# Optimization experiments

Measured on AMD Instinct MI355X. Metric: run time of the kernel, lower is better.

Reference implementation:

```python
import jax, jax.numpy as jnp
import numpy as np

B, N, D = 4, 2048, 1024
H = 16
E = D // H  # 64


def setup_inputs() -> dict:
    key = jax.random.key(0)
    k1, k2, k3 = jax.random.split(key, 3)
    x = jax.random.normal(k1, (B, N, D), dtype=jnp.float32)
    W_qkv = jax.random.normal(k2, (D, 3 * D), dtype=jnp.float32) * 0.02
    W_o = jax.random.normal(k3, (D, D), dtype=jnp.float32) * 0.02
    return {"x": x, "W_qkv": W_qkv, "W_o": W_o}


def reference(x, W_qkv, W_o):
    b, n, d = x.shape
    # QKV projection, then split as 'b n (3 heads e) -> 3 b heads n e'
    qkv = (x @ W_qkv).reshape(b, n, 3, H, E)
    qkv = jnp.transpose(qkv, (2, 0, 3, 1, 4))  # [3, b, H, n, E]
    q, k, v = qkv[0], qkv[1], qkv[2]
    # scores[i, j] = k_i . q_j / sqrt(E)  (note: rows indexed by k-pos, cols by q-pos, as in original)
    scores = jnp.einsum('bhie,bhje->bhij', k, q) / jnp.sqrt(jnp.asarray(E, dtype=x.dtype))
    # original masks strictly-lower-triangular (i > j) entries to -inf
    keep = jnp.triu(jnp.ones((n, n), dtype=bool))  # True where i <= j
    scores = jnp.where(keep, scores, -jnp.inf)
    attn = jax.nn.softmax(scores, axis=-1)  # softmax over last (q/v) axis, as in original
    out = jnp.einsum('bhij,bhje->bhie', attn, v)  # [b, H, n, E]
    out = jnp.transpose(out, (0, 2, 1, 3)).reshape(b, n, H * E)
    return out @ W_o
```

## Files before the change

### kernel.cpp

```cpp
#include <hip/hip_runtime.h>

typedef unsigned short u16;
typedef __bf16 bf16x8 __attribute__((ext_vector_type(8)));
typedef float f32x4 __attribute__((ext_vector_type(4)));
typedef unsigned short u16x8 __attribute__((ext_vector_type(8)));

__device__ inline u16 f2bf(float f) {
  unsigned u = __builtin_bit_cast(unsigned, f);
  u += 0x7fff + ((u >> 16) & 1);
  return (u16)(u >> 16);
}

__device__ inline f32x4 mfma16(bf16x8 a, bf16x8 b, f32x4 c) {
  return __builtin_amdgcn_mfma_f32_16x16x32_bf16(a, b, c, 0, 0, 0);
}

__global__ __launch_bounds__(256) void k_convert(const float* __restrict__ in,
                                                 u16* __restrict__ out, int n8) {
  int i = blockIdx.x * 256 + threadIdx.x;
  if (i >= n8) return;
  const float4* p = (const float4*)in + 2 * (size_t)i;
  float4 a = p[0], b = p[1];
  u16x8 v;
  v[0] = f2bf(a.x); v[1] = f2bf(a.y); v[2] = f2bf(a.z); v[3] = f2bf(a.w);
  v[4] = f2bf(b.x); v[5] = f2bf(b.y); v[6] = f2bf(b.z); v[7] = f2bf(b.w);
  *((u16x8*)out + i) = v;
}

__global__ __launch_bounds__(256) void k_transpose_conv(const float* __restrict__ in,
                                                        u16* __restrict__ out, int R, int C) {
  __shared__ float t[32][33];
  int c0 = blockIdx.x * 32, r0 = blockIdx.y * 32;
  int lx = threadIdx.x, ly = threadIdx.y;
#pragma unroll
  for (int i = 0; i < 32; i += 8)
    t[ly + i][lx] = in[(size_t)(r0 + ly + i) * C + c0 + lx];
  __syncthreads();
#pragma unroll
  for (int i = 0; i < 32; i += 8)
    out[(size_t)(c0 + ly + i) * R + r0 + lx] = f2bf(t[lx][ly + i]);
}

__global__ __launch_bounds__(256) void k_transpose_v(const u16* __restrict__ V,
                                                     u16* __restrict__ Vt) {
  __shared__ u16 t[64][72];
  int bh = blockIdx.y, n0 = blockIdx.x * 64;
  int tid = threadIdx.x;
  const u16* src = V + (size_t)bh * 2048 * 64;
  u16* dst = Vt + (size_t)bh * 64 * 2048;
#pragma unroll
  for (int half = 0; half < 2; ++half) {
    int f = half * 2048 + tid * 8;
    int r = f >> 6, e = f & 63;
    *(u16x8*)&t[r][e] = *(const u16x8*)&src[(size_t)(n0 + r) * 64 + e];
  }
  __syncthreads();
#pragma unroll
  for (int half = 0; half < 2; ++half) {
    int f = half * 2048 + tid * 8;
    int e = f >> 6, c = f & 63;
    u16x8 v;
#pragma unroll
    for (int j = 0; j < 8; ++j) v[j] = t[c + j][e];
    *(u16x8*)&dst[(size_t)e * 2048 + n0 + c] = v;
  }
}

template <int EPI>
__global__ __launch_bounds__(256) void k_gemm(const u16* __restrict__ A,
                                              const u16* __restrict__ Bt,
                                              void* __restrict__ o0, void* __restrict__ o1,
                                              void* __restrict__ o2, int M, int N, int K) {
  __shared__ u16 Al[2][128 * 40];
  __shared__ u16 Bl[2][128 * 40];
  const int tid = threadIdx.x, lane = tid & 63;
  const int row0 = blockIdx.x * 128, col0 = blockIdx.y * 128;
  const int w = tid >> 6;
  const int wr = (w >> 1) * 64, wc = (w & 1) * 64;
  const int srow = tid >> 2, skk = (tid & 3) * 8;
  const int l15 = lane & 15, lk = (lane >> 4) * 8;
  const int NK = K >> 5;
  f32x4 acc[4][4] = {};
  u16x8 ra0, ra1, rb0, rb1;
  const u16* ap0 = A + (size_t)(row0 + srow) * K + skk;
  const u16* bp0 = Bt + (size_t)(col0 + srow) * K + skk;

#define GLOAD(kt)                                              \
  do {                                                         \
    const u16* ap = ap0 + (size_t)(kt) * 32;                   \
    ra0 = *(const u16x8*)ap;                                   \
    ra1 = *(const u16x8*)(ap + (size_t)64 * K);                \
    const u16* bp = bp0 + (size_t)(kt) * 32;                   \
    rb0 = *(const u16x8*)bp;                                   \
    rb1 = *(const u16x8*)(bp + (size_t)64 * K);                \
  } while (0)
#define SWRITE(buf)                                            \
  do {                                                         \
    *(u16x8*)&Al[buf][srow * 40 + skk] = ra0;                  \
    *(u16x8*)&Al[buf][(64 + srow) * 40 + skk] = ra1;           \
    *(u16x8*)&Bl[buf][srow * 40 + skk] = rb0;                  \
    *(u16x8*)&Bl[buf][(64 + srow) * 40 + skk] = rb1;           \
  } while (0)

  GLOAD(0);
  SWRITE(0);
  int cur = 0;
  for (int kt = 0; kt < NK; ++kt) {
    __syncthreads();
    if (kt + 1 < NK) GLOAD(kt + 1);
    bf16x8 af[4], bfr[4];
#pragma unroll
    for (int m = 0; m < 4; ++m)
      af[m] = *(const bf16x8*)&Al[cur][(wr + m * 16 + l15) * 40 + lk];
#pragma unroll
    for (int n = 0; n < 4; ++n)
      bfr[n] = *(const bf16x8*)&Bl[cur][(wc + n * 16 + l15) * 40 + lk];
#pragma unroll
    for (int m = 0; m < 4; ++m)
#pragma unroll
      for (int n = 0; n < 4; ++n) acc[m][n] = mfma16(af[m], bfr[n], acc[m][n]);
    if (kt + 1 < NK) {
      SWRITE(cur ^ 1);
      cur ^= 1;
    }
  }
#undef GLOAD
#undef SWRITE
#pragma unroll
  for (int m = 0; m < 4; ++m)
#pragma unroll
    for (int n = 0; n < 4; ++n)
#pragma unroll
      for (int r = 0; r < 4; ++r) {
        int gr = row0 + wr + m * 16 + (lane >> 4) * 4 + r;
        int gc = col0 + wc + n * 16 + l15;
        float v = acc[m][n][r];
        if (EPI == 0) {
          int t = gc >> 10, rem = gc & 1023;
          int h = rem >> 6, e = rem & 63;
          int b = gr >> 11, nn = gr & 2047;
          if (t == 1) v *= 0.18033688011112042f;
          u16* dst = (t == 0) ? (u16*)o0 : (t == 1) ? (u16*)o1 : (u16*)o2;
          dst[((size_t)(b * 16 + h) * 2048 + nn) * 64 + e] = f2bf(v);
        } else {
          ((float*)o0)[(size_t)gr * N + gc] = v;
        }
      }
}

__global__ __launch_bounds__(256, 4) void k_attn(const u16* __restrict__ Kg,
                                                 const u16* __restrict__ Qg,
                                                 const u16* __restrict__ Vtg,
                                                 u16* __restrict__ Og) {
  __shared__ u16 Kq[64][72];
  __shared__ u16 Vt[64][72];
  __shared__ u16 Pl[4][32][80];
  const int tid = threadIdx.x, lane = tid & 63, w = tid >> 6;
  const int l15 = lane & 15, lg = lane >> 4;
  const int r0 = (15 - (int)blockIdx.x) * 128;
  const int bh = blockIdx.y;
  const int wrow = r0 + w * 32;
  const size_t base = (size_t)bh * 2048 * 64;

  bf16x8 qf[2][2];
#pragma unroll
  for (int i0 = 0; i0 < 2; ++i0)
#pragma unroll
    for (int kk = 0; kk < 2; ++kk)
      qf[i0][kk] = *(const bf16x8*)&Kg[base + (size_t)(wrow + i0 * 16 + l15) * 64 + kk * 32 + lg * 8];

  f32x4 acc[2][4] = {};
  float s_part[2][4] = {};

  const int srow = tid >> 2;
  const int scol = (tid & 3) * 16;
  const u16* kp = Qg + base + (size_t)srow * 64 + scol;
  const u16* vp = Vtg + base + (size_t)srow * 2048 + scol;

  u16x8 kr0, kr1, vr0, vr1;
  kr0 = *(const u16x8*)(kp + (size_t)r0 * 64);
  kr1 = *(const u16x8*)(kp + (size_t)r0 * 64 + 8);
  vr0 = *(const u16x8*)(vp + r0);
  vr1 = *(const u16x8*)(vp + r0 + 8);

  for (int j0 = r0; j0 < 2048; j0 += 64) {
    __syncthreads();
    *(u16x8*)&Kq[srow][scol] = kr0;
    *(u16x8*)&Kq[srow][scol + 8] = kr1;
    *(u16x8*)&Vt[srow][scol] = vr0;
    *(u16x8*)&Vt[srow][scol + 8] = vr1;
    __syncthreads();
    int jn = (j0 + 64 < 2048) ? j0 + 64 : j0;
    kr0 = *(const u16x8*)(kp + (size_t)jn * 64);
    kr1 = *(const u16x8*)(kp + (size_t)jn * 64 + 8);
    vr0 = *(const u16x8*)(vp + jn);
    vr1 = *(const u16x8*)(vp + jn + 8);

    if (j0 + 63 < wrow) continue;
    const bool diag = (j0 < wrow + 32);

    f32x4 S[2][4];
#pragma unroll
    for (int jf = 0; jf < 4; ++jf) {
      bf16x8 kf0 = *(const bf16x8*)&Kq[jf * 16 + l15][lg * 8];
      bf16x8 kf1 = *(const bf16x8*)&Kq[jf * 16 + l15][32 + lg * 8];
#pragma unroll
      for (int i0 = 0; i0 < 2; ++i0) {
        f32x4 z = {};
        z = mfma16(qf[i0][0], kf0, z);
        z = mfma16(qf[i0][1], kf1, z);
        S[i0][jf] = z;
      }
    }

#pragma unroll
    for (int i0 = 0; i0 < 2; ++i0)
#pragma unroll
      for (int r = 0; r < 4; ++r) {
        int gi = wrow + i0 * 16 + lg * 4 + r;
        float p0 = __builtin_amdgcn_exp2f(S[i0][0][r]);
        float p1 = __builtin_amdgcn_exp2f(S[i0][1][r]);
        float p2 = __builtin_amdgcn_exp2f(S[i0][2][r]);
        float p3 = __builtin_amdgcn_exp2f(S[i0][3][r]);
        if (diag) {
          p0 = (j0 + l15 >= gi) ? p0 : 0.f;
          p1 = (j0 + 16 + l15 >= gi) ? p1 : 0.f;
          p2 = (j0 + 32 + l15 >= gi) ? p2 : 0.f;
          p3 = (j0 + 48 + l15 >= gi) ? p3 : 0.f;
        }
        s_part[i0][r] += (p0 + p1) + (p2 + p3);
        u16* prow = &Pl[w][i0 * 16 + lg * 4 + r][l15];
        prow[0] = f2bf(p0);
        prow[16] = f2bf(p1);
        prow[32] = f2bf(p2);
        prow[48] = f2bf(p3);
      }

    bf16x8 pa[2][2];
#pragma unroll
    for (int i0 = 0; i0 < 2; ++i0) {
      pa[i0][0] = *(const bf16x8*)&Pl[w][i0 * 16 + l15][lg * 8];
      pa[i0][1] = *(const bf16x8*)&Pl[w][i0 * 16 + l15][32 + lg * 8];
    }
#pragma unroll
    for (int ef = 0; ef < 4; ++ef) {
      bf16x8 vb0 = *(const bf16x8*)&Vt[ef * 16 + l15][lg * 8];
      bf16x8 vb1 = *(const bf16x8*)&Vt[ef * 16 + l15][32 + lg * 8];
#pragma unroll
      for (int i0 = 0; i0 < 2; ++i0) {
        acc[i0][ef] = mfma16(pa[i0][0], vb0, acc[i0][ef]);
        acc[i0][ef] = mfma16(pa[i0][1], vb1, acc[i0][ef]);
      }
    }
  }

#pragma unroll
  for (int i0 = 0; i0 < 2; ++i0)
#pragma unroll
    for (int r = 0; r < 4; ++r) {
      float s = s_part[i0][r];
#pragma unroll
      for (int d = 1; d < 16; d <<= 1) s += __shfl_xor(s, d);
      s_part[i0][r] = 1.0f / s;
    }
  const size_t obase = ((size_t)(bh >> 4) * 2048) * 1024 + (size_t)(bh & 15) * 64;
#pragma unroll
  for (int i0 = 0; i0 < 2; ++i0)
#pragma unroll
    for (int ef = 0; ef < 4; ++ef)
#pragma unroll
      for (int r = 0; r < 4; ++r) {
        int gi = wrow + i0 * 16 + lg * 4 + r;
        Og[obase + (size_t)gi * 1024 + ef * 16 + l15] = f2bf(acc[i0][ef][r] * s_part[i0][r]);
      }
}

extern "C" void kernel_launch(void* const* d_in, const int* in_sizes, int n_in,
                              void* d_out, int out_size, void* d_ws, size_t ws_size,
                              hipStream_t stream) {
  const float* x = (const float*)d_in[0];
  const float* Wqkv = (const float*)d_in[1];
  const float* Wo = (const float*)d_in[2];
  char* ws = (char*)d_ws;
  u16* x_bf = (u16*)(ws);
  u16* Wq_t = (u16*)(ws + 16777216);
  u16* Wo_t = (u16*)(ws + 23068672);
  u16* Q = (u16*)(ws + 25165824);
  u16* Kx = (u16*)(ws + 41943040);
  u16* V = (u16*)(ws + 58720256);
  u16* Vt = (u16*)(ws + 75497472);
  u16* O = (u16*)(ws + 92274688);

  k_convert<<<8192 * 1024 / 8 / 256, 256, 0, stream>>>(x, x_bf, 8192 * 1024 / 8);
  k_transpose_conv<<<dim3(3072 / 32, 1024 / 32), dim3(32, 8), 0, stream>>>(Wqkv, Wq_t, 1024, 3072);
  k_transpose_conv<<<dim3(1024 / 32, 1024 / 32), dim3(32, 8), 0, stream>>>(Wo, Wo_t, 1024, 1024);
  k_gemm<0><<<dim3(64, 24), 256, 0, stream>>>(x_bf, Wq_t, Q, Kx, V, 8192, 3072, 1024);
  k_transpose_v<<<dim3(32, 64), 256, 0, stream>>>(V, Vt);
  k_attn<<<dim3(16, 64), 256, 0, stream>>>(Kx, Q, Vt, O);
  k_gemm<1><<<dim3(64, 8), 256, 0, stream>>>(O, Wo_t, d_out, nullptr, nullptr, 8192, 1024, 1024);
}
```

Baseline: 290.7 us.

## Use async global-to-LDS loads in GEMM and vectorize permuted P stores in attention

The GEMM staging now uses global_load_lds to copy A/B tiles straight into unpadded LDS buffers, replacing the register round-trip and the separate LDS write step. The attention kernel stores P as packed 4-element vectors in a permuted column order. The V transpose kernel applies the matching permutation so the PV product is unchanged. The causal row-block order is also remapped per (batch, head) to spread long and short blocks across the GPU. Dropping the LDS row padding in the GEMM may add bank conflicts on the MFMA fragment reads.

After: 290.2 us. No clear change (-0.2%).

```diff
diff --git a/kernel.cpp b/kernel.cpp
--- a/kernel.cpp
+++ b/kernel.cpp
@@ -3,6 +3,7 @@
 typedef unsigned short u16;
 typedef __bf16 bf16x8 __attribute__((ext_vector_type(8)));
 typedef float f32x4 __attribute__((ext_vector_type(4)));
+typedef unsigned short u16x4 __attribute__((ext_vector_type(4)));
 typedef unsigned short u16x8 __attribute__((ext_vector_type(8)));
 
 __device__ inline u16 f2bf(float f) {
@@ -13,6 +14,11 @@
 
 __device__ inline f32x4 mfma16(bf16x8 a, bf16x8 b, f32x4 c) {
   return __builtin_amdgcn_mfma_f32_16x16x32_bf16(a, b, c, 0, 0, 0);
+}
+
+__device__ inline void async16(const u16* g, u16* l) {
+  __builtin_amdgcn_global_load_lds((const __attribute__((address_space(1))) void*)g,
+                                   (__attribute__((address_space(3))) void*)l, 16, 0, 0);
 }
 
 __global__ __launch_bounds__(256) void k_convert(const float* __restrict__ in,
@@ -61,7 +67,10 @@
     int e = f >> 6, c = f & 63;
     u16x8 v;
 #pragma unroll
-    for (int j = 0; j < 8; ++j) v[j] = t[c + j][e];
+    for (int j = 0; j < 8; ++j) {
+      int tt = c + j;
+      v[j] = t[16 * (tt & 3) + (tt >> 2)][e];
+    }
     *(u16x8*)&dst[(size_t)e * 2048 + n0 + c] = v;
   }
 }
@@ -71,61 +80,47 @@
                                               const u16* __restrict__ Bt,
                                               void* __restrict__ o0, void* __restrict__ o1,
                                               void* __restrict__ o2, int M, int N, int K) {
-  __shared__ u16 Al[2][128 * 40];
-  __shared__ u16 Bl[2][128 * 40];
+  __shared__ u16 Al[2][128 * 32];
+  __shared__ u16 Bl[2][128 * 32];
   const int tid = threadIdx.x, lane = tid & 63;
   const int row0 = blockIdx.x * 128, col0 = blockIdx.y * 128;
   const int w = tid >> 6;
   const int wr = (w >> 1) * 64, wc = (w & 1) * 64;
-  const int srow = tid >> 2, skk = (tid & 3) * 8;
   const int l15 = lane & 15, lk = (lane >> 4) * 8;
   const int NK = K >> 5;
   f32x4 acc[4][4] = {};
-  u16x8 ra0, ra1, rb0, rb1;
-  const u16* ap0 = A + (size_t)(row0 + srow) * K + skk;
-  const u16* bp0 = Bt + (size_t)(col0 + srow) * K + skk;
-
-#define GLOAD(kt)                                              \
-  do {                                                         \
-    const u16* ap = ap0 + (size_t)(kt) * 32;                   \
-    ra0 = *(const u16x8*)ap;                                   \
-    ra1 = *(const u16x8*)(ap + (size_t)64 * K);                \
-    const u16* bp = bp0 + (size_t)(kt) * 32;                   \
-    rb0 = *(const u16x8*)bp;                                   \
-    rb1 = *(const u16x8*)(bp + (size_t)64 * K);                \
+  const u16* ap0 = A + (size_t)(row0 + (tid >> 2)) * K + (tid & 3) * 8;
+  const u16* bp0 = Bt + (size_t)(col0 + (tid >> 2)) * K + (tid & 3) * 8;
+
+#define STAGE(kt, buf)                                       \
+  do {                                                       \
+    const u16* as = ap0 + (size_t)(kt) * 32;                 \
+    const u16* bs = bp0 + (size_t)(kt) * 32;                 \
+    async16(as, &Al[buf][tid * 8]);                          \
+    async16(as + (size_t)64 * K, &Al[buf][2048 + tid * 8]);  \
+    async16(bs, &Bl[buf][tid * 8]);                          \
+    async16(bs + (size_t)64 * K, &Bl[buf][2048 + tid * 8]);  \
   } while (0)
-#define SWRITE(buf)                                            \
-  do {                                                         \
-    *(u16x8*)&Al[buf][srow * 40 + skk] = ra0;                  \
-    *(u16x8*)&Al[buf][(64 + srow) * 40 + skk] = ra1;           \
-    *(u16x8*)&Bl[buf][srow * 40 + skk] = rb0;                  \
-    *(u16x8*)&Bl[buf][(64 + srow) * 40 + skk] = rb1;           \
-  } while (0)
-
-  GLOAD(0);
-  SWRITE(0);
+
+  STAGE(0, 0);
   int cur = 0;
   for (int kt = 0; kt < NK; ++kt) {
     __syncthreads();
-    if (kt + 1 < NK) GLOAD(kt + 1);
+    if (kt + 1 < NK) STAGE(kt + 1, cur ^ 1);
     bf16x8 af[4], bfr[4];
 #pragma unroll
     for (int m = 0; m < 4; ++m)
-      af[m] = *(const bf16x8*)&Al[cur][(wr + m * 16 + l15) * 40 + lk];
+      af[m] = *(const bf16x8*)&Al[cur][(wr + m * 16 + l15) * 32 + lk];
 #pragma unroll
     for (int n = 0; n < 4; ++n)
-      bfr[n] = *(const bf16x8*)&Bl[cur][(wc + n * 16 + l15) * 40 + lk];
+      bfr[n] = *(const bf16x8*)&Bl[cur][(wc + n * 16 + l15) * 32 + lk];
 #pragma unroll
     for (int m = 0; m < 4; ++m)
 #pragma unroll
       for (int n = 0; n < 4; ++n) acc[m][n] = mfma16(af[m], bfr[n], acc[m][n]);
-    if (kt + 1 < NK) {
-      SWRITE(cur ^ 1);
-      cur ^= 1;
-    }
-  }
-#undef GLOAD
-#undef SWRITE
+    cur ^= 1;
+  }
+#undef STAGE
 #pragma unroll
   for (int m = 0; m < 4; ++m)
 #pragma unroll
@@ -154,11 +149,12 @@
                                                  u16* __restrict__ Og) {
   __shared__ u16 Kq[64][72];
   __shared__ u16 Vt[64][72];
-  __shared__ u16 Pl[4][32][80];
+  __shared__ u16 Pl[4][32][72];
   const int tid = threadIdx.x, lane = tid & 63, w = tid >> 6;
   const int l15 = lane & 15, lg = lane >> 4;
-  const int r0 = (15 - (int)blockIdx.x) * 128;
-  const int bh = blockIdx.y;
+  const int bx = blockIdx.x, by = blockIdx.y;
+  const int r0 = ((bx + 4 * (by >> 4)) & 15) * 128;
+  const int bh = by;
   const int wrow = r0 + w * 32;
   const size_t base = (size_t)bh * 2048 * 64;
 
@@ -229,11 +225,9 @@
           p3 = (j0 + 48 + l15 >= gi) ? p3 : 0.f;
         }
         s_part[i0][r] += (p0 + p1) + (p2 + p3);
-        u16* prow = &Pl[w][i0 * 16 + lg * 4 + r][l15];
-        prow[0] = f2bf(p0);
-        prow[16] = f2bf(p1);
-        prow[32] = f2bf(p2);
-        prow[48] = f2bf(p3);
+        u16x4 pk;
+        pk[0] = f2bf(p0); pk[1] = f2bf(p1); pk[2] = f2bf(p2); pk[3] = f2bf(p3);
+        *(u16x4*)&Pl[w][i0 * 16 + lg * 4 + r][4 * l15] = pk;
       }
 
     bf16x8 pa[2][2];
```
